# Optimization experiments

Hardware: AMD Instinct MI355X
Metric: run time of the kernel (lower is better)

## Reference

```python
import jax, jax.numpy as jnp
import numpy as np

HEADS = 12
EMBED = 768
HEAD_DIM = EMBED // HEADS


def setup_inputs() -> dict:
    key = jax.random.key(0)
    kx, kw, kb = jax.random.split(key, 3)
    x = jax.random.normal(kx, (8, 1024, EMBED), dtype=jnp.float32)
    # nn.Linear(embed, 3*embed): weight (3E, E), bias (3E,)
    W_qkv = jax.random.normal(kw, (3 * EMBED, EMBED), dtype=jnp.float32) * (1.0 / np.sqrt(EMBED))
    b_qkv = jax.random.normal(kb, (3 * EMBED,), dtype=jnp.float32) * 0.01
    return {"x": x, "W_qkv": W_qkv, "b_qkv": b_qkv}


def reference(x, W_qkv, b_qkv):
    b, n, e = x.shape
    qkv = x @ W_qkv.T + b_qkv                       # (b, n, 3E)
    qkv = qkv.reshape(b, n, HEADS, 3 * HEAD_DIM)    # (b, n, h, 3d)
    q, k, v = jnp.split(qkv, 3, axis=-1)            # each (b, n, h, d)
    scores = jnp.einsum('bihd,bjhd->bijh', q, k) / np.sqrt(HEAD_DIM)
    attn = jax.nn.softmax(scores, axis=-2)          # softmax over keys j (dim=-2)
    out = jnp.einsum('bijh,bjhd->bihd', attn, v)
    return out.reshape(b, n, e)
```

## Files before the change

kernel.cpp:

```cpp
#include <hip/hip_runtime.h>
#include <hip/hip_bf16.h>
#include <cstdint>
#include <math.h>

#define BATCH 8
#define SEQ   1024
#define EMB   768
#define HEADS 12
#define HDIM  64
#define C3    2304
#define MROWS (BATCH*SEQ)
#define NKT   (EMB / 32)
#define MTILES (MROWS / 128)
#define NTILES (C3 / 128)
#define XPACK_BLOCKS (MTILES * NKT)
#define WPACK_BLOCKS (NTILES * NKT)

typedef __attribute__((ext_vector_type(8)))  short bf16x8;
typedef __attribute__((ext_vector_type(4)))  short bf16x4;
typedef __attribute__((ext_vector_type(4)))  float f32x4;

static __device__ inline short f2bf(float f) {
    union { float f; uint32_t u; } v; v.f = f;
    uint32_t u = v.u + 0x7fff + ((v.u >> 16) & 1);
    return (short)(u >> 16);
}

static __device__ __forceinline__ void gload_lds16(const short* g, short* l) {
    __builtin_amdgcn_global_load_lds(
        (const __attribute__((address_space(1))) unsigned int*)g,
        (__attribute__((address_space(3))) unsigned int*)l, 16, 0, 0);
}

__global__ __launch_bounds__(256) void pack_bf16(const float* __restrict__ x,
                                                 short* __restrict__ xb2,
                                                 const float* __restrict__ W,
                                                 short* __restrict__ Wb2) {
    const float* in;
    short* out;
    int blk;
    if (blockIdx.x < XPACK_BLOCKS) {
        in = x; out = xb2; blk = blockIdx.x;
    } else {
        in = W; out = Wb2; blk = blockIdx.x - XPACK_BLOCKS;
    }
    const int mt = blk / NKT;
    const int kt = blk % NKT;
    short* obase = out + (size_t)blk * 4096;

    #pragma unroll
    for (int p = 0; p < 2; ++p) {
        int idx = p * 256 + threadIdx.x;
        int r = idx >> 2, s = idx & 3;
        const float* src = in + (size_t)(mt * 128 + r) * EMB + kt * 32 + s * 8;
        float4 v0 = ((const float4*)src)[0];
        float4 v1 = ((const float4*)src)[1];
        bf16x8 o = { f2bf(v0.x), f2bf(v0.y), f2bf(v0.z), f2bf(v0.w),
                     f2bf(v1.x), f2bf(v1.y), f2bf(v1.z), f2bf(v1.w) };
        int S = ((4 * r + s) ^ (r & 7));
        *(bf16x8*)(obase + S * 8) = o;
    }
}

#define LVP 136

__global__ __launch_bounds__(256) void qkv_gemm_mfma(const short* __restrict__ Apk,
                                                     const short* __restrict__ Bpk,
                                                     const float* __restrict__ bias,
                                                     short* __restrict__ qkvb,
                                                     short* __restrict__ vt) {
    __shared__ short smem[16384];
    short (*As)[4096] = (short (*)[4096])smem;
    short (*Bs)[4096] = (short (*)[4096])(smem + 8192);
    short* Lv = smem;

    const int g    = blockIdx.x;
    const int xcd  = g & 7;
    const int ring = g >> 3;
    const int by   = xcd * 8 + (ring & 7);
    const int bx   = ring >> 3;

    const int t    = threadIdx.x;
    const int w    = t >> 6;
    const int lane = t & 63;
    const int s4   = lane >> 4;
    const int r15  = lane & 15;
    const int m0 = by * 128, n0 = bx * 128;
    const int wm = (w & 1) * 64, wn = (w >> 1) * 64;

    const short* Ab = Apk + (size_t)by * (NKT * 4096);
    const short* Bb = Bpk + (size_t)bx * (NKT * 4096);

    int offA[4], offB[4];
    #pragma unroll
    for (int i = 0; i < 4; ++i) {
        int ra = wm + i * 16 + r15;
        offA[i] = ((4 * ra + s4) ^ (ra & 7)) << 3;
        int rb = wn + i * 16 + r15;
        offB[i] = ((4 * rb + s4) ^ (rb & 7)) << 3;
    }

    const int seg0 = w * 2;

#define STAGE(buf, kt) do {                                                   \
        const short* _a = Ab + (size_t)(kt) * 4096;                           \
        const short* _b = Bb + (size_t)(kt) * 4096;                           \
        gload_lds16(_a + (seg0    ) * 512 + lane * 8, &As[buf][(seg0    ) * 512]); \
        gload_lds16(_b + (seg0    ) * 512 + lane * 8, &Bs[buf][(seg0    ) * 512]); \
        gload_lds16(_a + (seg0 + 1) * 512 + lane * 8, &As[buf][(seg0 + 1) * 512]); \
        gload_lds16(_b + (seg0 + 1) * 512 + lane * 8, &Bs[buf][(seg0 + 1) * 512]); \
    } while (0)

#define LOAD_FRAGS(buf)                                                       \
        _Pragma("unroll")                                                     \
        for (int i = 0; i < 4; ++i) {                                         \
            af[i]  = *(const bf16x8*)&As[buf][offA[i]];                       \
            bff[i] = *(const bf16x8*)&Bs[buf][offB[i]];                       \
        }

#define MFMA16()                                                              \
        __builtin_amdgcn_s_setprio(1);                                        \
        _Pragma("unroll")                                                     \
        for (int mi = 0; mi < 4; ++mi)                                        \
            _Pragma("unroll")                                                 \
            for (int ni = 0; ni < 4; ++ni)                                    \
                acc[mi][ni] = __builtin_amdgcn_mfma_f32_16x16x32_bf16(        \
                    af[mi], bff[ni], acc[mi][ni], 0, 0, 0);                   \
        __builtin_amdgcn_s_setprio(0);

    f32x4 acc[4][4] = {};
    bf16x8 af[4], bff[4];

    STAGE(0, 0);
    STAGE(1, 1);
    asm volatile("s_waitcnt vmcnt(4)" ::: "memory");
    __builtin_amdgcn_s_barrier();

    for (int tt = 0; tt < NKT - 2; ++tt) {
        const int buf = tt & 1;
        LOAD_FRAGS(buf);
        asm volatile("s_waitcnt lgkmcnt(0)" ::: "memory");
        __builtin_amdgcn_sched_barrier(0);
        __builtin_amdgcn_s_barrier();
        STAGE(buf, tt + 2);
        MFMA16();
        asm volatile("s_waitcnt vmcnt(4)" ::: "memory");
        __builtin_amdgcn_s_barrier();
    }
    {
        LOAD_FRAGS((NKT - 2) & 1);
        asm volatile("s_waitcnt lgkmcnt(0)" ::: "memory");
        __builtin_amdgcn_sched_barrier(0);
        __builtin_amdgcn_s_barrier();
        MFMA16();
        asm volatile("s_waitcnt vmcnt(0)" ::: "memory");
        __builtin_amdgcn_s_barrier();
    }
    {
        LOAD_FRAGS((NKT - 1) & 1);
        asm volatile("s_waitcnt lgkmcnt(0)" ::: "memory");
        __builtin_amdgcn_sched_barrier(0);
        __builtin_amdgcn_s_barrier();
        MFMA16();
    }
#undef STAGE
#undef LOAD_FRAGS
#undef MFMA16

    const int bxm   = bx % 3;
    const bool has_v    = (bxm != 0);
    const int  wn_v     = (bxm == 1) ? 0 : 64;
    const bool is_vwave = has_v && (wn == wn_v);

    float bsv[4], scl[4];
    #pragma unroll
    for (int ni = 0; ni < 4; ++ni) {
        int n = n0 + wn + ni * 16 + r15;
        bsv[ni] = bias[n];
        scl[ni] = ((n % 192) < 64) ? 0.125f : 1.0f;
    }

    if (!is_vwave) {
        #pragma unroll
        for (int mi = 0; mi < 4; ++mi) {
            const int m = m0 + wm + mi * 16 + s4 * 4;
            #pragma unroll
            for (int ni = 0; ni < 4; ++ni) {
                const int n = n0 + wn + ni * 16 + r15;
                #pragma unroll
                for (int reg = 0; reg < 4; ++reg)
                    qkvb[(size_t)(m + reg) * C3 + n] =
                        f2bf((acc[mi][ni][reg] + bsv[ni]) * scl[ni]);
            }
        }
    } else {
        #pragma unroll
        for (int mi = 0; mi < 4; ++mi) {
            const int jl = wm + mi * 16 + s4 * 4;
            #pragma unroll
            for (int ni = 0; ni < 4; ++ni) {
                const int d = ni * 16 + r15;
                bf16x4 vv = { f2bf(acc[mi][ni][0] + bsv[ni]),
                              f2bf(acc[mi][ni][1] + bsv[ni]),
                              f2bf(acc[mi][ni][2] + bsv[ni]),
                              f2bf(acc[mi][ni][3] + bsv[ni]) };
                *(bf16x4*)&Lv[d * LVP + jl] = vv;
            }
        }
    }

    if (has_v) {
        __syncthreads();
        const int h  = (n0 + wn_v) / 192;
        const int bb = by >> 3;
        const int j0 = m0 & 1023;
        short* vrow = vt + ((size_t)(bb * HEADS + h) * 64) * SEQ + j0;
        #pragma unroll
        for (int p = 0; p < 4; ++p) {
            int lin = p * 256 + t;
            int d   = lin >> 4;
            int ch  = lin & 15;
            *(bf16x8*)(vrow + (size_t)d * SEQ + ch * 8) =
                *(bf16x8*)&Lv[d * LVP + ch * 8];
        }
    }
}

__global__ __launch_bounds__(256, 4) void attn_mfma(const short* __restrict__ qkvb,
                                                    const short* __restrict__ vt,
                                                    float* __restrict__ out) {
    __shared__ short Ks[64][64];
    __shared__ short Vt[64][64];
    __shared__ short Ps[64][64];

    const int g    = blockIdx.x;
    const int qt   = g / (BATCH * HEADS);
    const int bh   = g % (BATCH * HEADS);
    const int b    = bh / HEADS;
    const int h    = bh % HEADS;
    const int t    = threadIdx.x;
    const int w    = t >> 6;
    const int lane = t & 63;
    const int c    = lane & 15;
    const int q    = lane >> 4;
    const int ck   = c & 7;
    const int i0   = qt * 64;

    const size_t base = (size_t)b * SEQ * C3 + (size_t)h * 192;
    const short* vtb = vt + (size_t)bh * 64 * SEQ;
    const short* gk  = qkvb + base + 64;

    bf16x8 aq0, aq1;
    {
        const short* pq = qkvb + base + (size_t)(i0 + w * 16 + c) * C3 + q * 8;
        aq0 = *(const bf16x8*)(pq);
        aq1 = *(const bf16x8*)(pq + 32);
    }

    const int jA = t >> 3;
    const int jB = jA + 32;
    const int sg = t & 7;
    const int wKA = (sg ^ (jA & 7)) * 8;
    const int wKB = (sg ^ (jB & 7)) * 8;

    bf16x8 kr0, kr1, vr0, vr1;
    kr0 = *(const bf16x8*)(gk + (size_t)jA * C3 + sg * 8);
    kr1 = *(const bf16x8*)(gk + (size_t)jB * C3 + sg * 8);
    vr0 = *(const bf16x8*)(vtb + (size_t)jA * SEQ + sg * 8);
    vr1 = *(const bf16x8*)(vtb + (size_t)jB * SEQ + sg * 8);

    f32x4 o[4] = {};
    float l_acc = 0.f;

    for (int kt = 0; kt < 16; ++kt) {
        __syncthreads();
        *(bf16x8*)&Ks[jA][wKA] = kr0;
        *(bf16x8*)&Ks[jB][wKB] = kr1;
        *(bf16x8*)&Vt[jA][wKA] = vr0;
        *(bf16x8*)&Vt[jB][wKB] = vr1;
        __syncthreads();

        if (kt < 15) {
            const int j0 = (kt + 1) * 64;
            kr0 = *(const bf16x8*)(gk + (size_t)(j0 + jA) * C3 + sg * 8);
            kr1 = *(const bf16x8*)(gk + (size_t)(j0 + jB) * C3 + sg * 8);
            vr0 = *(const bf16x8*)(vtb + (size_t)jA * SEQ + j0 + sg * 8);
            vr1 = *(const bf16x8*)(vtb + (size_t)jB * SEQ + j0 + sg * 8);
        }

        bf16x8 ka[4][2];
        #pragma unroll
        for (int mt = 0; mt < 4; ++mt) {
            ka[mt][0] = *(bf16x8*)&Ks[mt * 16 + c][(q ^ ck) * 8];
            ka[mt][1] = *(bf16x8*)&Ks[mt * 16 + c][((4 + q) ^ ck) * 8];
        }

        f32x4 s[4];
        __builtin_amdgcn_s_setprio(1);
        #pragma unroll
        for (int mt = 0; mt < 4; ++mt) {
            f32x4 acc = {0.f, 0.f, 0.f, 0.f};
            acc = __builtin_amdgcn_mfma_f32_16x16x32_bf16(ka[mt][0], aq0, acc, 0, 0, 0);
            acc = __builtin_amdgcn_mfma_f32_16x16x32_bf16(ka[mt][1], aq1, acc, 0, 0, 0);
            s[mt] = acc;
        }
        __builtin_amdgcn_s_setprio(0);

        #pragma unroll
        for (int mt = 0; mt < 4; ++mt) {
            float p0 = __expf(s[mt][0]);
            float p1 = __expf(s[mt][1]);
            float p2 = __expf(s[mt][2]);
            float p3 = __expf(s[mt][3]);
            l_acc += (p0 + p1) + (p2 + p3);
            bf16x4 pw = { f2bf(p0), f2bf(p1), f2bf(p2), f2bf(p3) };
            int pcol = (((2 * mt + (q >> 1)) ^ ck) << 3) + (q & 1) * 4;
            *(bf16x4*)&Ps[w * 16 + c][pcol] = pw;
        }

        bf16x8 vb[4][2];
        #pragma unroll
        for (int dt = 0; dt < 4; ++dt) {
            vb[dt][0] = *(bf16x8*)&Vt[dt * 16 + c][(q ^ ck) * 8];
            vb[dt][1] = *(bf16x8*)&Vt[dt * 16 + c][((4 + q) ^ ck) * 8];
        }

        bf16x8 ap0 = *(bf16x8*)&Ps[w * 16 + c][(q ^ ck) * 8];
        bf16x8 ap1 = *(bf16x8*)&Ps[w * 16 + c][((4 + q) ^ ck) * 8];
        __builtin_amdgcn_s_setprio(1);
        #pragma unroll
        for (int dt = 0; dt < 4; ++dt) {
            o[dt] = __builtin_amdgcn_mfma_f32_16x16x32_bf16(ap0, vb[dt][0], o[dt], 0, 0, 0);
            o[dt] = __builtin_amdgcn_mfma_f32_16x16x32_bf16(ap1, vb[dt][1], o[dt], 0, 0, 0);
        }
        __builtin_amdgcn_s_setprio(0);
    }

    float v = l_acc;
    v += __shfl_xor(v, 16, 64);
    v += __shfl_xor(v, 32, 64);
    float linv[4];
    #pragma unroll
    for (int r = 0; r < 4; ++r)
        linv[r] = 1.0f / __shfl(v, 4 * q + r, 64);

    #pragma unroll
    for (int dt = 0; dt < 4; ++dt)
        #pragma unroll
        for (int r = 0; r < 4; ++r) {
            int i = w * 16 + q * 4 + r;
            out[((size_t)b * SEQ + i0 + i) * EMB + h * HDIM + dt * 16 + c]
                = o[dt][r] * linv[r];
        }
}

extern "C" void kernel_launch(void* const* d_in, const int* in_sizes, int n_in,
                              void* d_out, int out_size, void* d_ws, size_t ws_size,
                              hipStream_t stream) {
    const float* x    = (const float*)d_in[0];
    const float* W    = (const float*)d_in[1];
    const float* bias = (const float*)d_in[2];
    float* out = (float*)d_out;

    short* xb2  = (short*)d_ws;
    short* Wb2  = xb2 + (size_t)MROWS * EMB;
    short* qkvb = Wb2 + (size_t)C3 * EMB;
    short* vt   = qkvb + (size_t)MROWS * C3;

    pack_bf16<<<XPACK_BLOCKS + WPACK_BLOCKS, 256, 0, stream>>>(x, xb2, W, Wb2);

    qkv_gemm_mfma<<<1152, 256, 0, stream>>>(xb2, Wb2, bias, qkvb, vt);

    attn_mfma<<<BATCH * HEADS * (SEQ / 64), 256, 0, stream>>>(qkvb, vt, out);
}
```

Before: 160.7 us.

## Double-buffer K/V tiles with direct global-to-LDS loads in attention kernel

The attention kernel previously staged K and V through registers, then wrote them to shared memory between two full block barriers each iteration. It now issues direct global-to-LDS loads into two shared-memory buffers, prefetching the tile two iterations ahead. It synchronises with vmcnt waits and raw s_barrier calls. The aim is to hide global load latency behind the MFMA work and drop the register round-trip, at the cost of doubling K/V shared-memory use (about 40KB per block), which may pressure occupancy.

```diff
diff --git a/kernel.cpp b/kernel.cpp
--- a/kernel.cpp
+++ b/kernel.cpp
@@ -229,8 +229,8 @@
 __global__ __launch_bounds__(256, 4) void attn_mfma(const short* __restrict__ qkvb,
                                                     const short* __restrict__ vt,
                                                     float* __restrict__ out) {
-    __shared__ short Ks[64][64];
-    __shared__ short Vt[64][64];
+    __shared__ short Ks[2][64][64];
+    __shared__ short Vt[2][64][64];
     __shared__ short Ps[64][64];
 
     const int g    = blockIdx.x;
@@ -257,42 +257,36 @@
         aq1 = *(const bf16x8*)(pq + 32);
     }
 
-    const int jA = t >> 3;
-    const int jB = jA + 32;
-    const int sg = t & 7;
-    const int wKA = (sg ^ (jA & 7)) * 8;
-    const int wKB = (sg ^ (jB & 7)) * 8;
-
-    bf16x8 kr0, kr1, vr0, vr1;
-    kr0 = *(const bf16x8*)(gk + (size_t)jA * C3 + sg * 8);
-    kr1 = *(const bf16x8*)(gk + (size_t)jB * C3 + sg * 8);
-    vr0 = *(const bf16x8*)(vtb + (size_t)jA * SEQ + sg * 8);
-    vr1 = *(const bf16x8*)(vtb + (size_t)jB * SEQ + sg * 8);
+    const int rloc  = lane >> 3;
+    const int chunk = (lane & 7) ^ rloc;
+    const short* srcK0 = gk  + (size_t)(16 * w + rloc)     * C3  + chunk * 8;
+    const short* srcK1 = gk  + (size_t)(16 * w + 8 + rloc) * C3  + chunk * 8;
+    const short* srcV0 = vtb + (size_t)(16 * w + rloc)     * SEQ + chunk * 8;
+    const short* srcV1 = vtb + (size_t)(16 * w + 8 + rloc) * SEQ + chunk * 8;
+
+#define STAGE(buf, j0g) do {                                                  \
+        gload_lds16(srcK0 + (size_t)(j0g) * C3, &Ks[buf][16 * w][0]);         \
+        gload_lds16(srcK1 + (size_t)(j0g) * C3, &Ks[buf][16 * w + 8][0]);     \
+        gload_lds16(srcV0 + (j0g),              &Vt[buf][16 * w][0]);         \
+        gload_lds16(srcV1 + (j0g),              &Vt[buf][16 * w + 8][0]);     \
+    } while (0)
 
     f32x4 o[4] = {};
     float l_acc = 0.f;
 
+    STAGE(0, 0);
+    STAGE(1, 64);
+    asm volatile("s_waitcnt vmcnt(4)" ::: "memory");
+    __builtin_amdgcn_s_barrier();
+
     for (int kt = 0; kt < 16; ++kt) {
-        __syncthreads();
-        *(bf16x8*)&Ks[jA][wKA] = kr0;
-        *(bf16x8*)&Ks[jB][wKB] = kr1;
-        *(bf16x8*)&Vt[jA][wKA] = vr0;
-        *(bf16x8*)&Vt[jB][wKB] = vr1;
-        __syncthreads();
-
-        if (kt < 15) {
-            const int j0 = (kt + 1) * 64;
-            kr0 = *(const bf16x8*)(gk + (size_t)(j0 + jA) * C3 + sg * 8);
-            kr1 = *(const bf16x8*)(gk + (size_t)(j0 + jB) * C3 + sg * 8);
-            vr0 = *(const bf16x8*)(vtb + (size_t)jA * SEQ + j0 + sg * 8);
-            vr1 = *(const bf16x8*)(vtb + (size_t)jB * SEQ + j0 + sg * 8);
-        }
+        const int cur = kt & 1;
 
         bf16x8 ka[4][2];
         #pragma unroll
         for (int mt = 0; mt < 4; ++mt) {
-            ka[mt][0] = *(bf16x8*)&Ks[mt * 16 + c][(q ^ ck) * 8];
-            ka[mt][1] = *(bf16x8*)&Ks[mt * 16 + c][((4 + q) ^ ck) * 8];
+            ka[mt][0] = *(bf16x8*)&Ks[cur][mt * 16 + c][(q ^ ck) * 8];
+            ka[mt][1] = *(bf16x8*)&Ks[cur][mt * 16 + c][((4 + q) ^ ck) * 8];
         }
 
         f32x4 s[4];
@@ -321,8 +315,8 @@
         bf16x8 vb[4][2];
         #pragma unroll
         for (int dt = 0; dt < 4; ++dt) {
-            vb[dt][0] = *(bf16x8*)&Vt[dt * 16 + c][(q ^ ck) * 8];
-            vb[dt][1] = *(bf16x8*)&Vt[dt * 16 + c][((4 + q) ^ ck) * 8];
+            vb[dt][0] = *(bf16x8*)&Vt[cur][dt * 16 + c][(q ^ ck) * 8];
+            vb[dt][1] = *(bf16x8*)&Vt[cur][dt * 16 + c][((4 + q) ^ ck) * 8];
         }
 
         bf16x8 ap0 = *(bf16x8*)&Ps[w * 16 + c][(q ^ ck) * 8];
@@ -334,7 +328,19 @@
             o[dt] = __builtin_amdgcn_mfma_f32_16x16x32_bf16(ap1, vb[dt][1], o[dt], 0, 0, 0);
         }
         __builtin_amdgcn_s_setprio(0);
-    }
+
+        if (kt < 15) {
+            __builtin_amdgcn_s_barrier();
+            if (kt < 14) {
+                STAGE(cur, (kt + 2) * 64);
+                asm volatile("s_waitcnt vmcnt(4)" ::: "memory");
+            } else {
+                asm volatile("s_waitcnt vmcnt(0)" ::: "memory");
+            }
+            __builtin_amdgcn_s_barrier();
+        }
+    }
+#undef STAGE
 
     float v = l_acc;
     v += __shfl_xor(v, 16, 64);
```

Result: no change. 162.0 us (+0.8%).
